# Kernel tuning notes

Hardware: AMD Instinct MI355X
Metric: run time of the kernel (lower is better)

The kernel has to match this reference:

```python
import jax, jax.numpy as jnp
import numpy as np

B, N, QD = 2, 2048, 1024
CTX_LEN, TCD = 77, 768
NUM_PROMPT, PD = 64, 1024
HEADS, DIM_HEAD = 8, 64
INNER = HEADS * DIM_HEAD  # 512
SCALE = DIM_HEAD ** -0.5


def setup_inputs() -> dict:
    key = jax.random.key(0)
    ks = jax.random.split(key, 10)
    s = lambda *sh: 1.0 / np.sqrt(sh[0])
    return {
        "x": jax.random.normal(ks[0], (B, N, QD), jnp.float32),
        "context": jax.random.normal(ks[1], (B, CTX_LEN, TCD), jnp.float32),
        "prompt": jax.random.normal(ks[2], (1, NUM_PROMPT, PD), jnp.float32),
        "w_prompt": jax.random.normal(ks[3], (PD, TCD), jnp.float32) * s(PD),
        "w_img": jax.random.normal(ks[4], (QD, TCD), jnp.float32) * s(QD),
        "w_q": jax.random.normal(ks[5], (QD, INNER), jnp.float32) * s(QD),
        "w_k": jax.random.normal(ks[6], (TCD, INNER), jnp.float32) * s(TCD),
        "w_v": jax.random.normal(ks[7], (TCD, INNER), jnp.float32) * s(TCD),
        "w_out": jax.random.normal(ks[8], (INNER, QD), jnp.float32) * s(INNER),
        "b_out": jax.random.normal(ks[9], (QD,), jnp.float32) * 0.01,
    }


def reference(x, context, prompt, w_prompt, w_img, w_q, w_k, w_v, w_out, b_out):
    b, n, _ = x.shape
    # q projection
    q = x @ w_q  # [B, N, INNER]
    # build kv context: [text ; projected prompt ; projected image tokens]
    prompt_ctx = jnp.broadcast_to(prompt @ w_prompt, (b, NUM_PROMPT, TCD))
    img_ctx = x @ w_img  # [B, N, TCD]
    ctx = jnp.concatenate([context, prompt_ctx, img_ctx], axis=1)  # [B, J, TCD]
    k = ctx @ w_k
    v = ctx @ w_v
    # split heads: [B, H, L, D]
    split = lambda t: t.reshape(b, t.shape[1], HEADS, DIM_HEAD).transpose(0, 2, 1, 3)
    qh, kh, vh = split(q), split(k), split(v)
    sim = jnp.einsum("bhid,bhjd->bhij", qh, kh) * SCALE
    attn = jax.nn.softmax(sim, axis=-1)
    out = jnp.einsum("bhij,bhjd->bhid", attn, vh)  # [B, H, N, D]
    out = out.transpose(0, 2, 1, 3).reshape(b, n, INNER)
    return out @ w_out + b_out
```

## Files before the change

kernel.cpp:

```cpp
#include <hip/hip_runtime.h>
#include <hip/hip_bf16.h>
#include <math.h>

#define BB 2
#define NN 2048
#define QD 1024
#define CTX_LEN 77
#define TCD 768
#define NUM_PROMPT 64
#define PD 1024
#define HEADS 8
#define DIM_HEAD 64
#define INNER 512
#define JTOT (CTX_LEN + NUM_PROMPT + NN)
#define SCALE 0.125f
#define SCALEL2 (0.125f * 1.44269504088896f)
#define MTOT (BB * NN)
#define JPAD 2240
#define KVPAD 2304
#define NT_J (JPAD / 64)

typedef unsigned short u16;
typedef unsigned int u32;
typedef __attribute__((ext_vector_type(8))) short bf16x8;
typedef __attribute__((ext_vector_type(4))) float f32x4;

__device__ __forceinline__ u32 pack_split(float f) {
  u32 u = __builtin_bit_cast(u32, f);
  u32 hi = u & 0xffff0000u;
  float lo = f - __builtin_bit_cast(float, hi);
  u32 ul = __builtin_bit_cast(u32, lo);
  return __builtin_amdgcn_perm(ul, u, 0x07060302u);
}
__device__ __forceinline__ void split2(float f, u16& h, u16& l) {
  u32 u = __builtin_bit_cast(u32, f);
  u32 hm = u & 0xffff0000u;
  float lo = f - __builtin_bit_cast(float, hm);
  h = (u16)(u >> 16);
  l = (u16)(__builtin_bit_cast(u32, lo) >> 16);
}
__device__ __forceinline__ u16 rnd_bf16(float f) {
  u32 u = __builtin_bit_cast(u32, f);
  return (u16)((u + 0x7FFF + ((u >> 16) & 1)) >> 16);
}
__device__ __forceinline__ ushort4 pack4r(const float4& f) {
  ushort4 r;
  r.x = rnd_bf16(f.x); r.y = rnd_bf16(f.y);
  r.z = rnd_bf16(f.z); r.w = rnd_bf16(f.w);
  return r;
}

template <int CTRL>
__device__ __forceinline__ float dpp_f(float x) {
  int i = __builtin_bit_cast(int, x);
  i = __builtin_amdgcn_update_dpp(0, i, CTRL, 0xF, 0xF, false);
  return __builtin_bit_cast(float, i);
}

__device__ __forceinline__ void gload16(const u16* g, u32* l) {
  __builtin_amdgcn_global_load_lds(
      (const __attribute__((address_space(1))) u32*)(const void*)g,
      (__attribute__((address_space(3))) u32*)(void*)l, 16, 0, 0);
}

__global__ __launch_bounds__(256) void pack_planes4(
    const float* __restrict__ s0, u16* __restrict__ d0, int n0,
    const float* __restrict__ s1, u16* __restrict__ d1, int n1,
    const float* __restrict__ ctx, u16* __restrict__ ch, int n2,
    u16* __restrict__ zh, int n3) {
  int i = blockIdx.x * 256 + threadIdx.x;
  if (i < n0) {
    ((ushort4*)d0)[i] = pack4r(((const float4*)s0)[i]);
    return;
  }
  i -= n0;
  if (i < n1) {
    ((ushort4*)d1)[i] = pack4r(((const float4*)s1)[i]);
    return;
  }
  i -= n1;
  if (i < n2) {
    ushort4 rr = pack4r(((const float4*)ctx)[i]);
    int c4 = i % (TCD / 4);
    int rb = i / (TCD / 4);
    int r = rb % CTX_LEN, b = rb / CTX_LEN;
    size_t o = ((size_t)b * JTOT + r) * (TCD / 4) + c4;
    ((ushort4*)ch)[o] = rr;
    return;
  }
  i -= n2;
  if (i >= n3) return;
  int c = i & 7;
  int row = i >> 3;
  int d = row & 511;
  int b = row >> 9;
  uint4 z = {0u, 0u, 0u, 0u};
  *(uint4*)&zh[((size_t)b * INNER + d) * KVPAD + 2176 + c * 8] = z;
}

struct TP6 {
  const float* src[6];
  u16* dh[6];
  u16* dl[6];
  int K[6], N[6];
  int blk0[7];
};

__global__ __launch_bounds__(256) void transpose_pack6(TP6 P) {
  __shared__ u32 T[32][33];
  const int bid = blockIdx.x;
  int s = 0;
#pragma unroll
  for (int k = 1; k < 6; ++k) s += (bid >= P.blk0[k]);
  const int rel = bid - P.blk0[s];
  const int N = P.N[s], K = P.K[s];
  const int nbx = N >> 5;
  const int bx = rel % nbx, by = rel / nbx;
  const float* __restrict__ src = P.src[s];
  u16* __restrict__ dh = P.dh[s];
  u16* __restrict__ dl = P.dl[s];
  const int t = threadIdx.x;
  const int k0 = by * 32, n0 = bx * 32;
#pragma unroll
  for (int i = 0; i < 4; ++i) {
    int e = t + i * 256;
    int kr = e >> 5, nc = e & 31;
    T[kr][nc] = pack_split(src[(size_t)(k0 + kr) * N + n0 + nc]);
  }
  __syncthreads();
#pragma unroll
  for (int i = 0; i < 4; ++i) {
    int e = t + i * 256;
    int nr = e >> 5, kc = e & 31;
    u32 w = T[kc][nr];
    size_t idx = (size_t)(n0 + nr) * K + k0 + kc;
    if (dl) {
      dh[idx] = (u16)(w & 0xffff);
      dl[idx] = (u16)(w >> 16);
    } else {
      dh[idx] = (u16)(w & 0xffff);
    }
  }
}

template <int MODE>
__global__ __launch_bounds__(256) void gemm_mfma(
    const u16* __restrict__ Agh, const u16* __restrict__ Agl,
    const u16* __restrict__ Bgh, const u16* __restrict__ Bgl,
    u16* __restrict__ O1h,
    u16* __restrict__ O2h,
    float* __restrict__ Of, const float* __restrict__ bias,
    int M, int K, int Ntot,
    const u16* __restrict__ A2h, const u16* __restrict__ B2h) {
  constexpr bool ONET = (MODE == 1 || MODE == 2);
  constexpr int ALSZ = ONET ? 4 : 2 * 128 * 16;
  constexpr int BLSZ = ONET ? 4 : 2 * 64 * 16;
  __shared__ __align__(16) u32 Ah_s[2][128 * 16];
  __shared__ __align__(16) u32 Al_s[ALSZ];
  __shared__ __align__(16) u32 Bh_s[2][64 * 16];
  __shared__ __align__(16) u32 Bl_s[BLSZ];

  int bxi = blockIdx.x, byi = blockIdx.y;
  {
    const int GX = gridDim.x;
    const int nwg = GX * gridDim.y;
    const int lid = byi * GX + bxi;
    const int qq = nwg >> 3, rr = nwg & 7;
    const int xcd = lid & 7, pos = lid >> 3;
    const int swz = (xcd < rr ? xcd * (qq + 1) : rr * (qq + 1) + (xcd - rr) * qq) + pos;
    bxi = swz % GX; byi = swz / GX;
  }
  const int bm = byi * 128, bn = bxi * 64;

  const bool pband = (MODE == 1) && (bm >= MTOT);
  if (pband && bn >= TCD) return;

  int b2 = 0, jbase = 0;
  if (MODE == 2) { b2 = (byi >= 18); jbase = (byi - b2 * 18) * 128; }

  const int t = threadIdx.x;
  const int w = t >> 6, lane = t & 63;
  const int m16 = lane & 15, quad = lane >> 4;
  const int wm = w >> 1, wn = w & 1;

  const u16* Abh = Agh; const u16* Abl = Agl;
  const u16* Bbh = Bgh; const u16* Bbl = Bgl;
  int rowlim = M - 1;
  int bmA = bm;
  if (pband) { Abh = A2h; Bbh = B2h; rowlim = NUM_PROMPT - 1; bmA = 0; }

  const int acol = (lane & 3) * 8;
  const int ar0 = 32 * w + (lane >> 2);
  const int ar1 = ar0 + 16;
  int ag0, ag1;
  if (MODE == 2) {
    ag0 = b2 * JTOT + min(jbase + ar0, JTOT - 1);
    ag1 = b2 * JTOT + min(jbase + ar1, JTOT - 1);
  } else {
    ag0 = min(bmA + ar0, rowlim);
    ag1 = min(bmA + ar1, rowlim);
  }
  const u16* a0h = Abh + (size_t)ag0 * K + acol;
  const u16* a1h = Abh + (size_t)ag1 * K + acol;
  const u16* a0l = ONET ? nullptr : Abl + (size_t)ag0 * K + acol;
  const u16* a1l = ONET ? nullptr : Abl + (size_t)ag1 * K + acol;
  const int br = 16 * w + (lane >> 2);
  const u16* b0h = Bbh + (size_t)(bn + br) * K + acol;
  const u16* b0l = ONET ? nullptr : Bbl + (size_t)(bn + br) * K + acol;

  f32x4 acc[4][2];
#pragma unroll
  for (int i = 0; i < 4; ++i)
#pragma unroll
    for (int j = 0; j < 2; ++j) acc[i][j] = (f32x4){0.f, 0.f, 0.f, 0.f};

  for (int k0 = 0; k0 < K; k0 += 64) {
#pragma unroll
    for (int s = 0; s < 2; ++s) {
      const int kc = k0 + s * 32;
      gload16(a0h + kc, &Ah_s[s][(2 * w) * 256]);
      gload16(a1h + kc, &Ah_s[s][(2 * w + 1) * 256]);
      gload16(b0h + kc, &Bh_s[s][w * 256]);
      if constexpr (!ONET) {
        gload16(a0l + kc, &Al_s[s * 2048 + (2 * w) * 256]);
        gload16(a1l + kc, &Al_s[s * 2048 + (2 * w + 1) * 256]);
        gload16(b0l + kc, &Bl_s[s * 1024 + w * 256]);
      }
    }
    __syncthreads();

#pragma unroll
    for (int s = 0; s < 2; ++s) {
      bf16x8 ah[4], al[4], bh[2], bl[2];
#pragma unroll
      for (int mt = 0; mt < 4; ++mt) {
        int off = (wm * 64 + mt * 16 + m16) * 16 + quad * 4;
        ah[mt] = *(const bf16x8*)&Ah_s[s][off];
        if constexpr (!ONET) al[mt] = *(const bf16x8*)&Al_s[s * 2048 + off];
      }
#pragma unroll
      for (int nt = 0; nt < 2; ++nt) {
        int off = (wn * 32 + nt * 16 + m16) * 16 + quad * 4;
        bh[nt] = *(const bf16x8*)&Bh_s[s][off];
        if constexpr (!ONET) bl[nt] = *(const bf16x8*)&Bl_s[s * 1024 + off];
      }
#pragma unroll
      for (int mt = 0; mt < 4; ++mt)
#pragma unroll
        for (int nt = 0; nt < 2; ++nt) {
          acc[mt][nt] = __builtin_amdgcn_mfma_f32_16x16x32_bf16(ah[mt], bh[nt], acc[mt][nt], 0, 0, 0);
          if constexpr (!ONET) {
            acc[mt][nt] = __builtin_amdgcn_mfma_f32_16x16x32_bf16(ah[mt], bl[nt], acc[mt][nt], 0, 0, 0);
            acc[mt][nt] = __builtin_amdgcn_mfma_f32_16x16x32_bf16(al[mt], bh[nt], acc[mt][nt], 0, 0, 0);
          }
        }
    }
    __syncthreads();
  }

  if (MODE == 2 && bn >= INNER) {
    u16* Th = (u16*)Ah_s;
#pragma unroll
    for (int mt = 0; mt < 4; ++mt)
#pragma unroll
      for (int nt = 0; nt < 2; ++nt)
#pragma unroll
        for (int r = 0; r < 4; ++r) {
          int dl = wn * 32 + nt * 16 + m16;
          int jl = wm * 64 + mt * 16 + quad * 4 + r;
          int adr = dl * 128 + ((((jl >> 3) ^ (dl & 15)) << 3) | (jl & 7));
          Th[adr] = rnd_bf16(acc[mt][nt][r]);
        }
    __syncthreads();
#pragma unroll
    for (int i = 0; i < 4; ++i) {
      int chunk = t + i * 256;
      int dl = chunk >> 4, jc = chunk & 15;
      int jg = jbase + jc * 8;
      int lofs = dl * 128 + ((jc ^ (dl & 15)) << 3);
      uint4 vh4 = *(const uint4*)&Th[lofs];
      size_t rowo = ((size_t)b2 * INNER + (bn - INNER) + dl) * KVPAD;
      if (jg + 8 <= JTOT) {
        *(uint4*)&O2h[rowo + jg] = vh4;
      } else if (jg < JTOT) {
        const u16* eh = (const u16*)&vh4;
#pragma unroll
        for (int e = 0; e < 8; ++e)
          if (jg + e < JTOT) O2h[rowo + jg + e] = eh[e];
      }
    }
    return;
  }

#pragma unroll
  for (int mt = 0; mt < 4; ++mt)
#pragma unroll
    for (int nt = 0; nt < 2; ++nt)
#pragma unroll
      for (int r = 0; r < 4; ++r) {
        int gm = bm + wm * 64 + mt * 16 + quad * 4 + r;
        int gn = bn + wn * 32 + nt * 16 + m16;
        float v = acc[mt][nt][r];
        if (MODE == 1) {
          if (pband) {
            int pr = wm * 64 + mt * 16 + quad * 4 + r;
            if (pr < NUM_PROMPT && gn < TCD) {
              u16 rv = rnd_bf16(v);
              O1h[((size_t)CTX_LEN + pr) * TCD + gn] = rv;
              O1h[((size_t)JTOT + CTX_LEN + pr) * TCD + gn] = rv;
            }
          } else if (gn < TCD) {
            size_t row = (size_t)(gm >> 11) * JTOT + 141 + (gm & 2047);
            O1h[row * TCD + gn] = rnd_bf16(v);
          } else {
            O2h[(size_t)gm * INNER + (gn - TCD)] = rnd_bf16(v * SCALEL2);
          }
        } else if (MODE == 2) {
          int jloc = jbase + wm * 64 + mt * 16 + quad * 4 + r;
          O1h[((size_t)b2 * KVPAD + jloc) * INNER + gn] = rnd_bf16(v);
        } else if (MODE == 3) {
          Of[(size_t)gm * QD + gn] = v + bias[gn];
        }
      }
}

__global__ __launch_bounds__(256) void attn_mfma2(
    const u16* __restrict__ qhg,
    const u16* __restrict__ khg,
    const u16* __restrict__ vtg_h,
    u16* __restrict__ aoh, u16* __restrict__ aol) {
  __shared__ __align__(16) u16 Kh_s[64 * 64];
  __shared__ __align__(16) u16 Vh_s[64 * 64];
  __shared__ __align__(16) u16 Ph_s[64 * 72];

  const int t = threadIdx.x;
  const int w = t >> 6, lane = t & 63;
  const int m16 = lane & 15, quad = lane >> 4;

  const int id = blockIdx.x;
  const int swz = (id & 7) * 64 + (id >> 3);
  const int qt = swz & 31, bh = swz >> 5;
  const int b = bh >> 3, h = bh & 7;
  const int qrow0 = qt * 64;

  bf16x8 qh[2];
  {
    size_t qoff = ((size_t)(b * NN + qrow0 + w * 16 + m16)) * INNER + h * 64 + quad * 8;
#pragma unroll
    for (int ks = 0; ks < 2; ++ks)
      qh[ks] = *(const bf16x8*)(qhg + qoff + ks * 32);
  }

  const int sr = lane >> 3;
  const int sc = (lane & 7) ^ sr;
  const int c0 = (w & 1) * 4;
  const u16* gp;
  u32* lp;
  size_t cstr, jstr;
  if (w < 2) {
    gp = khg + ((size_t)b * KVPAD + c0 * 8 + sr) * INNER + h * 64 + sc * 8;
    lp = (u32*)Kh_s + c0 * 256;
    cstr = (size_t)8 * INNER;
    jstr = (size_t)64 * INNER;
  } else {
    gp = vtg_h + ((size_t)b * INNER + h * 64 + c0 * 8 + sr) * KVPAD + sc * 8;
    lp = (u32*)Vh_s + c0 * 256;
    cstr = (size_t)8 * KVPAD;
    jstr = 64;
  }

  f32x4 O[4] = {{0.f,0.f,0.f,0.f},{0.f,0.f,0.f,0.f},{0.f,0.f,0.f,0.f},{0.f,0.f,0.f,0.f}};
  float lpart[4];
#pragma unroll
  for (int r = 0; r < 4; ++r) lpart[r] = 0.f;

  for (int tile = 0; tile < NT_J; ++tile) {
    const int j0 = tile * 64;
    __syncthreads();
#pragma unroll
    for (int c = 0; c < 4; ++c) gload16(gp + (size_t)c * cstr, lp + c * 256);
    gp += jstr;
    __syncthreads();

    f32x4 S[4];
    __builtin_amdgcn_s_setprio(1);
#pragma unroll
    for (int jt = 0; jt < 4; ++jt) {
      const int row = jt * 16 + m16;
      f32x4 acc = {0.f, 0.f, 0.f, 0.f};
#pragma unroll
      for (int ks = 0; ks < 2; ++ks) {
        const int cc = row * 64 + (((ks * 4 + quad) ^ (row & 7)) << 3);
        bf16x8 kh = *(const bf16x8*)&Kh_s[cc];
        acc = __builtin_amdgcn_mfma_f32_16x16x32_bf16(qh[ks], kh, acc, 0, 0, 0);
      }
      S[jt] = acc;
    }
    __builtin_amdgcn_s_setprio(0);

#pragma unroll
    for (int jt = 0; jt < 4; ++jt) {
      int jc = j0 + jt * 16 + m16;
      if (jc >= JTOT)
#pragma unroll
        for (int r = 0; r < 4; ++r) S[jt][r] = -INFINITY;
    }

    float pj[4][4];
#pragma unroll
    for (int jt = 0; jt < 4; ++jt)
#pragma unroll
      for (int r = 0; r < 4; ++r) {
        float pv = __builtin_amdgcn_exp2f(S[jt][r] - 8.f);
        pj[jt][r] = pv;
        lpart[r] += pv;
      }

#pragma unroll
    for (int jt = 0; jt < 4; ++jt)
#pragma unroll
      for (int r = 0; r < 4; ++r) {
        int pq = (w * 16 + quad * 4 + r) * 72 + jt * 16 + m16;
        Ph_s[pq] = rnd_bf16(pj[jt][r]);
      }

    bf16x8 ph[2];
#pragma unroll
    for (int ks = 0; ks < 2; ++ks) {
      int po = (w * 16 + m16) * 72 + ks * 32 + quad * 8;
      ph[ks] = *(const bf16x8*)&Ph_s[po];
    }

    __builtin_amdgcn_s_setprio(1);
#pragma unroll
    for (int nt = 0; nt < 4; ++nt) {
      const int row = nt * 16 + m16;
#pragma unroll
      for (int ks = 0; ks < 2; ++ks) {
        const int cc = row * 64 + (((ks * 4 + quad) ^ (row & 7)) << 3);
        bf16x8 vh = *(const bf16x8*)&Vh_s[cc];
        O[nt] = __builtin_amdgcn_mfma_f32_16x16x32_bf16(ph[ks], vh, O[nt], 0, 0, 0);
      }
    }
    __builtin_amdgcn_s_setprio(0);
  }

  float inv[4];
#pragma unroll
  for (int r = 0; r < 4; ++r) {
    float rs = lpart[r];
    rs += dpp_f<0xB1>(rs);
    rs += dpp_f<0x4E>(rs);
    rs += dpp_f<0x124>(rs);
    rs += dpp_f<0x128>(rs);
    inv[r] = 1.f / rs;
  }
#pragma unroll
  for (int nt = 0; nt < 4; ++nt)
#pragma unroll
    for (int r = 0; r < 4; ++r) {
      size_t idx = ((size_t)(b * NN + qrow0 + w * 16 + quad * 4 + r)) * INNER +
                   h * 64 + nt * 16 + m16;
      u16 sh, sl;
      split2(O[nt][r] * inv[r], sh, sl);
      aoh[idx] = sh; aol[idx] = sl;
    }
}

extern "C" void kernel_launch(void* const* d_in, const int* in_sizes, int n_in,
                              void* d_out, int out_size, void* d_ws, size_t ws_size,
                              hipStream_t stream) {
  const float* x        = (const float*)d_in[0];
  const float* context  = (const float*)d_in[1];
  const float* prompt   = (const float*)d_in[2];
  const float* w_prompt = (const float*)d_in[3];
  const float* w_img    = (const float*)d_in[4];
  const float* w_q      = (const float*)d_in[5];
  const float* w_k      = (const float*)d_in[6];
  const float* w_v      = (const float*)d_in[7];
  const float* w_out    = (const float*)d_in[8];
  const float* b_out    = (const float*)d_in[9];
  float* out = (float*)d_out;

  const int M = MTOT;
  const int MJ = BB * JTOT;

  u16* p = (u16*)d_ws;
  const size_t qN = (size_t)M * INNER;
  const size_t ctxN = (size_t)MJ * TCD;
  const size_t kN = (size_t)BB * KVPAD * INNER;
  u16* cth = p; p += ctxN;
  u16* aoh = p; p += qN;   u16* aol = p; p += qN;
  u16* xh  = p; p += (size_t)M * QD;
  u16* prh = p; p += (size_t)NUM_PROMPT * PD;
  u16* WtPh = p; p += (size_t)TCD * PD;
  u16* WtAh = p; p += (size_t)(TCD + INNER) * QD;
  u16* WtBh = p; p += (size_t)(2 * INNER) * TCD;
  u16* WtOh = p; p += (size_t)QD * INNER;          u16* WtOl = p; p += (size_t)QD * INNER;
  u16* qhp = p; p += qN;
  u16* khp = p; p += kN;
  u16* vthp = p; p += kN;

  const int n4x = M * QD / 4, n4p = NUM_PROMPT * PD / 4;
  const int n4c = BB * CTX_LEN * TCD / 4;
  const int n4z = BB * INNER * 8;
  pack_planes4<<<(n4x + n4p + n4c + n4z + 255) / 256, 256, 0, stream>>>(
      x, xh, n4x, prompt, prh, n4p, context, cth, n4c, vthp, n4z);

  TP6 tp;
  const float* srcs[6] = {w_prompt, w_img, w_q, w_k, w_v, w_out};
  u16* dhs[6] = {WtPh, WtAh, WtAh + (size_t)TCD * QD, WtBh, WtBh + (size_t)INNER * TCD, WtOh};
  u16* dls[6] = {nullptr, nullptr, nullptr, nullptr, nullptr, WtOl};
  int Ks[6] = {PD, QD, QD, TCD, TCD, INNER};
  int Ns[6] = {TCD, TCD, INNER, INNER, INNER, QD};
  int acc_blk = 0;
  for (int i = 0; i < 6; ++i) {
    tp.src[i] = srcs[i]; tp.dh[i] = dhs[i]; tp.dl[i] = dls[i];
    tp.K[i] = Ks[i]; tp.N[i] = Ns[i];
    tp.blk0[i] = acc_blk;
    acc_blk += (Ns[i] / 32) * (Ks[i] / 32);
  }
  tp.blk0[6] = acc_blk;
  transpose_pack6<<<acc_blk, 256, 0, stream>>>(tp);

  gemm_mfma<1><<<dim3((TCD + INNER) / 64, M / 128 + 1), 256, 0, stream>>>(
      xh, nullptr, WtAh, nullptr, cth, qhp, nullptr, nullptr,
      M, QD, TCD + INNER, prh, WtPh);
  gemm_mfma<2><<<dim3((2 * INNER) / 64, 2 * (KVPAD / 128)), 256, 0, stream>>>(
      cth, nullptr, WtBh, nullptr, khp, vthp, nullptr, nullptr,
      MJ, TCD, 2 * INNER, nullptr, nullptr);
  attn_mfma2<<<BB * HEADS * (NN / 64), 256, 0, stream>>>(
      qhp, khp, vthp, aoh, aol);
  gemm_mfma<3><<<dim3(QD / 64, M / 128), 256, 0, stream>>>(
      aoh, aol, WtOh, WtOl, nullptr, nullptr, out, b_out,
      M, INNER, QD, nullptr, nullptr);
}
```

Measured before the change: 198.9 us.

## Double-buffer K/V shared tiles in attention to overlap loads with MFMA

Gives the attention kernel's K and V shared-memory tiles two buffers. The next tile's global-to-LDS load is issued before computing on the current one, and a partial vmcnt wait replaces the pair of __syncthreads. The goal is to hide global load latency behind the QK and PV MFMA work. The padding mask is also skipped on all tiles except the last partial one. The cost is twice the K/V LDS footprint, which could lower occupancy, plus reliance on hand-placed waitcnt and barrier ordering for correctness.

```diff
diff --git a/kernel.cpp b/kernel.cpp
--- a/kernel.cpp
+++ b/kernel.cpp
@@ -329,8 +329,8 @@
     const u16* __restrict__ khg,
     const u16* __restrict__ vtg_h,
     u16* __restrict__ aoh, u16* __restrict__ aol) {
-  __shared__ __align__(16) u16 Kh_s[64 * 64];
-  __shared__ __align__(16) u16 Vh_s[64 * 64];
+  __shared__ __align__(16) u16 Kh_s[2][64 * 64];
+  __shared__ __align__(16) u16 Vh_s[2][64 * 64];
   __shared__ __align__(16) u16 Ph_s[64 * 72];
 
   const int t = threadIdx.x;
@@ -355,16 +355,16 @@
   const int sc = (lane & 7) ^ sr;
   const int c0 = (w & 1) * 4;
   const u16* gp;
-  u32* lp;
+  u32* lp0;
   size_t cstr, jstr;
   if (w < 2) {
     gp = khg + ((size_t)b * KVPAD + c0 * 8 + sr) * INNER + h * 64 + sc * 8;
-    lp = (u32*)Kh_s + c0 * 256;
+    lp0 = (u32*)Kh_s + c0 * 256;
     cstr = (size_t)8 * INNER;
     jstr = (size_t)64 * INNER;
   } else {
     gp = vtg_h + ((size_t)b * INNER + h * 64 + c0 * 8 + sr) * KVPAD + sc * 8;
-    lp = (u32*)Vh_s + c0 * 256;
+    lp0 = (u32*)Vh_s + c0 * 256;
     cstr = (size_t)8 * KVPAD;
     jstr = 64;
   }
@@ -374,13 +374,23 @@
 #pragma unroll
   for (int r = 0; r < 4; ++r) lpart[r] = 0.f;
 
+#pragma unroll
+  for (int c = 0; c < 4; ++c) gload16(gp + (size_t)c * cstr, lp0 + c * 256);
+  gp += jstr;
+
   for (int tile = 0; tile < NT_J; ++tile) {
     const int j0 = tile * 64;
-    __syncthreads();
-#pragma unroll
-    for (int c = 0; c < 4; ++c) gload16(gp + (size_t)c * cstr, lp + c * 256);
-    gp += jstr;
-    __syncthreads();
+    const int cur = tile & 1;
+    {
+      u32* dst = lp0 + (cur ^ 1) * 2048;
+#pragma unroll
+      for (int c = 0; c < 4; ++c) gload16(gp + (size_t)c * cstr, dst + c * 256);
+      gp += jstr;
+    }
+    asm volatile("s_waitcnt vmcnt(4)" ::: "memory");
+    __builtin_amdgcn_s_barrier();
+    const u16* Kc = Kh_s[cur];
+    const u16* Vc = Vh_s[cur];
 
     f32x4 S[4];
     __builtin_amdgcn_s_setprio(1);
@@ -391,19 +401,21 @@
 #pragma unroll
       for (int ks = 0; ks < 2; ++ks) {
         const int cc = row * 64 + (((ks * 4 + quad) ^ (row & 7)) << 3);
-        bf16x8 kh = *(const bf16x8*)&Kh_s[cc];
+        bf16x8 kh = *(const bf16x8*)&Kc[cc];
         acc = __builtin_amdgcn_mfma_f32_16x16x32_bf16(qh[ks], kh, acc, 0, 0, 0);
       }
       S[jt] = acc;
     }
     __builtin_amdgcn_s_setprio(0);
 
-#pragma unroll
-    for (int jt = 0; jt < 4; ++jt) {
-      int jc = j0 + jt * 16 + m16;
-      if (jc >= JTOT)
-#pragma unroll
-        for (int r = 0; r < 4; ++r) S[jt][r] = -INFINITY;
+    if (j0 + 64 > JTOT) {
+#pragma unroll
+      for (int jt = 0; jt < 4; ++jt) {
+        int jc = j0 + jt * 16 + m16;
+        if (jc >= JTOT)
+#pragma unroll
+          for (int r = 0; r < 4; ++r) S[jt][r] = -INFINITY;
+      }
     }
 
     float pj[4][4];
@@ -438,12 +450,15 @@
 #pragma unroll
       for (int ks = 0; ks < 2; ++ks) {
         const int cc = row * 64 + (((ks * 4 + quad) ^ (row & 7)) << 3);
-        bf16x8 vh = *(const bf16x8*)&Vh_s[cc];
+        bf16x8 vh = *(const bf16x8*)&Vc[cc];
         O[nt] = __builtin_amdgcn_mfma_f32_16x16x32_bf16(ph[ks], vh, O[nt], 0, 0, 0);
       }
     }
     __builtin_amdgcn_s_setprio(0);
-  }
+    __builtin_amdgcn_s_barrier();
+  }
+
+  asm volatile("s_waitcnt vmcnt(0)" ::: "memory");
 
   float inv[4];
 #pragma unroll
```

Measured after the change: 195.8 us. No clear change (-1.6%).

## Split attention over two key ranges and merge partials in a combine kernel

Applied to the files above, without the earlier changes.

Each attention block now covers half of the key tiles, which doubles the grid from 512 to 1024 blocks so more of the GPU's compute units are busy. Unnormalized fp32 partial outputs and row sums go to a workspace, and a new combine kernel adds the two halves, normalizes, and writes the hi/lo bf16 planes. The padding mask now runs only on the last partial tile. In exchange it adds fp32 partial-output traffic and an extra kernel launch. Merging without a max rescale is safe because both halves already use the same fixed exp offset.

```diff
diff --git a/kernel.cpp b/kernel.cpp
--- a/kernel.cpp
+++ b/kernel.cpp
@@ -19,6 +19,7 @@
 #define JPAD 2240
 #define KVPAD 2304
 #define NT_J (JPAD / 64)
+#define NT_SPLIT 18
 
 typedef unsigned short u16;
 typedef unsigned int u32;
@@ -328,7 +329,7 @@
     const u16* __restrict__ qhg,
     const u16* __restrict__ khg,
     const u16* __restrict__ vtg_h,
-    u16* __restrict__ aoh, u16* __restrict__ aol) {
+    float* __restrict__ Opart, float* __restrict__ lsum) {
   __shared__ __align__(16) u16 Kh_s[64 * 64];
   __shared__ __align__(16) u16 Vh_s[64 * 64];
   __shared__ __align__(16) u16 Ph_s[64 * 72];
@@ -338,10 +339,14 @@
   const int m16 = lane & 15, quad = lane >> 4;
 
   const int id = blockIdx.x;
-  const int swz = (id & 7) * 64 + (id >> 3);
-  const int qt = swz & 31, bh = swz >> 5;
+  const int swz = (id & 7) * 128 + (id >> 3);
+  const int jh = swz & 1;
+  const int qt = (swz >> 1) & 31;
+  const int bh = swz >> 6;
   const int b = bh >> 3, h = bh & 7;
   const int qrow0 = qt * 64;
+  const int t0 = jh ? NT_SPLIT : 0;
+  const int t1 = jh ? NT_J : NT_SPLIT;
 
   bf16x8 qh[2];
   {
@@ -358,12 +363,12 @@
   u32* lp;
   size_t cstr, jstr;
   if (w < 2) {
-    gp = khg + ((size_t)b * KVPAD + c0 * 8 + sr) * INNER + h * 64 + sc * 8;
+    gp = khg + ((size_t)b * KVPAD + t0 * 64 + c0 * 8 + sr) * INNER + h * 64 + sc * 8;
     lp = (u32*)Kh_s + c0 * 256;
     cstr = (size_t)8 * INNER;
     jstr = (size_t)64 * INNER;
   } else {
-    gp = vtg_h + ((size_t)b * INNER + h * 64 + c0 * 8 + sr) * KVPAD + sc * 8;
+    gp = vtg_h + ((size_t)b * INNER + h * 64 + c0 * 8 + sr) * KVPAD + t0 * 64 + sc * 8;
     lp = (u32*)Vh_s + c0 * 256;
     cstr = (size_t)8 * KVPAD;
     jstr = 64;
@@ -374,7 +379,7 @@
 #pragma unroll
   for (int r = 0; r < 4; ++r) lpart[r] = 0.f;
 
-  for (int tile = 0; tile < NT_J; ++tile) {
+  for (int tile = t0; tile < t1; ++tile) {
     const int j0 = tile * 64;
     __syncthreads();
 #pragma unroll
@@ -398,12 +403,14 @@
     }
     __builtin_amdgcn_s_setprio(0);
 
-#pragma unroll
-    for (int jt = 0; jt < 4; ++jt) {
-      int jc = j0 + jt * 16 + m16;
-      if (jc >= JTOT)
-#pragma unroll
-        for (int r = 0; r < 4; ++r) S[jt][r] = -INFINITY;
+    if (j0 + 64 > JTOT) {
+#pragma unroll
+      for (int jt = 0; jt < 4; ++jt) {
+        int jc = j0 + jt * 16 + m16;
+        if (jc >= JTOT)
+#pragma unroll
+          for (int r = 0; r < 4; ++r) S[jt][r] = -INFINITY;
+      }
     }
 
     float pj[4][4];
@@ -445,7 +452,7 @@
     __builtin_amdgcn_s_setprio(0);
   }
 
-  float inv[4];
+  float lres[4];
 #pragma unroll
   for (int r = 0; r < 4; ++r) {
     float rs = lpart[r];
@@ -453,18 +460,47 @@
     rs += dpp_f<0x4E>(rs);
     rs += dpp_f<0x124>(rs);
     rs += dpp_f<0x128>(rs);
-    inv[r] = 1.f / rs;
+    lres[r] = rs;
+  }
+  if (m16 == 0) {
+#pragma unroll
+    for (int r = 0; r < 4; ++r) {
+      size_t row = (size_t)b * NN + qrow0 + w * 16 + quad * 4 + r;
+      lsum[((size_t)jh * MTOT + row) * HEADS + h] = lres[r];
+    }
   }
 #pragma unroll
   for (int nt = 0; nt < 4; ++nt)
 #pragma unroll
     for (int r = 0; r < 4; ++r) {
-      size_t idx = ((size_t)(b * NN + qrow0 + w * 16 + quad * 4 + r)) * INNER +
+      size_t idx = ((size_t)jh * MTOT + b * NN + qrow0 + w * 16 + quad * 4 + r) * INNER +
                    h * 64 + nt * 16 + m16;
-      u16 sh, sl;
-      split2(O[nt][r] * inv[r], sh, sl);
-      aoh[idx] = sh; aol[idx] = sl;
-    }
+      Opart[idx] = O[nt][r];
+    }
+}
+
+__global__ __launch_bounds__(256) void combine_attn(
+    const float* __restrict__ Opart, const float* __restrict__ lsum,
+    u16* __restrict__ aoh, u16* __restrict__ aol) {
+  int i = blockIdx.x * 256 + threadIdx.x;
+  const int total4 = MTOT * INNER / 4;
+  if (i >= total4) return;
+  int row = i / (INNER / 4);
+  int c4 = (i % (INNER / 4)) * 4;
+  int h = c4 >> 6;
+  float4 o0 = ((const float4*)Opart)[i];
+  float4 o1 = ((const float4*)(Opart + (size_t)MTOT * INNER))[i];
+  float l = lsum[(size_t)row * HEADS + h] + lsum[((size_t)MTOT + row) * HEADS + h];
+  float inv = 1.f / l;
+  float v0 = (o0.x + o1.x) * inv;
+  float v1 = (o0.y + o1.y) * inv;
+  float v2 = (o0.z + o1.z) * inv;
+  float v3 = (o0.w + o1.w) * inv;
+  ushort4 hh, ll;
+  split2(v0, hh.x, ll.x); split2(v1, hh.y, ll.y);
+  split2(v2, hh.z, ll.z); split2(v3, hh.w, ll.w);
+  ((ushort4*)aoh)[i] = hh;
+  ((ushort4*)aol)[i] = ll;
 }
 
 extern "C" void kernel_launch(void* const* d_in, const int* in_sizes, int n_in,
@@ -500,6 +536,8 @@
   u16* qhp = p; p += qN;
   u16* khp = p; p += kN;
   u16* vthp = p; p += kN;
+  float* Opart = (float*)p; p += 2 * qN * 2;
+  float* lsum  = (float*)p; p += (size_t)2 * MTOT * HEADS * 2;
 
   const int n4x = M * QD / 4, n4p = NUM_PROMPT * PD / 4;
   const int n4c = BB * CTX_LEN * TCD / 4;
@@ -529,8 +567,10 @@
   gemm_mfma<2><<<dim3((2 * INNER) / 64, 2 * (KVPAD / 128)), 256, 0, stream>>>(
       cth, nullptr, WtBh, nullptr, khp, vthp, nullptr, nullptr,
       MJ, TCD, 2 * INNER, nullptr, nullptr);
-  attn_mfma2<<<BB * HEADS * (NN / 64), 256, 0, stream>>>(
-      qhp, khp, vthp, aoh, aol);
+  attn_mfma2<<<BB * HEADS * (NN / 64) * 2, 256, 0, stream>>>(
+      qhp, khp, vthp, Opart, lsum);
+  combine_attn<<<(M * INNER / 4 + 255) / 256, 256, 0, stream>>>(
+      Opart, lsum, aoh, aol);
   gemm_mfma<3><<<dim3(QD / 64, M / 128), 256, 0, stream>>>(
       aoh, aol, WtOh, WtOl, nullptr, nullptr, out, b_out,
       M, INNER, QD, nullptr, nullptr);
```

Result: no change. 195.2 us (median of 2 runs) (-1.9%).
